# Optimization experiments

Hardware: AMD Instinct MI355X
Metric: run time of the kernel (lower is better)

The kernel has to match this reference:

```python
import jax, jax.numpy as jnp
import numpy as np

B, DIM = 32768, 768
M, K = 128, 32          # num_subvectors, code_size
D = DIM // M            # subvector_dim = 6


def setup_inputs() -> dict:
    key = jax.random.key(0)
    kx, kc = jax.random.split(key)
    x = jax.random.normal(kx, (B, DIM), dtype=jnp.float32)
    codebooks = jax.random.normal(kc, (M, K, D), dtype=jnp.float32) * 0.01
    return {"x": x, "codebooks": codebooks}


def reference(x, codebooks):
    b = x.shape[0]
    m, k, d = codebooks.shape
    sub = x.reshape(b, m, d)                                   # (B, M, D)
    # per-subvector dot products with each code: (B, M, K)
    dots = jnp.einsum('bmd,mkd->bmk', sub, codebooks)
    soft = jax.nn.softmax(dots, axis=2)                        # (B, M, K)
    soft_q = jnp.einsum('bmk,mkd->bmd', soft, codebooks)       # (B, M, D)
    idx = jnp.argmax(dots, axis=2)                             # (B, M) int
    discrete = codebooks[jnp.arange(m)[None, :], idx]          # (B, M, D)
    # straight-through: forward = discrete, gradient flows through soft_q
    quant = soft_q - jax.lax.stop_gradient(soft_q - discrete)
    return quant.reshape(b, m * d)
```

## Files before the change

kernel.cpp:

```cpp
#include <hip/hip_runtime.h>
#include <float.h>


typedef float v2f __attribute__((ext_vector_type(2)));

#define BATCH 32768
#define DIM   768
#define K_CB  32
#define D_SUB 6
#define BROWS 16
#define RSTG  8
#define NSTG  (BROWS/RSTG)
#define HALFF 384
#define STGF  (RSTG*HALFF)

#define DPP_XOR1 0xB1
#define DPP_XOR2 0x4E

template<int CTRL>
__device__ __forceinline__ float dppf(float v) {
    return __int_as_float(__builtin_amdgcn_update_dpp(
        0, __float_as_int(v), CTRL, 0xF, 0xF, true));
}
template<int CTRL>
__device__ __forceinline__ int dppi(int v) {
    return __builtin_amdgcn_update_dpp(0, v, CTRL, 0xF, 0xF, true);
}

__global__ __launch_bounds__(256, 4)
void pq_head_kernel(const float* __restrict__ x,
                    const float* __restrict__ cb,
                    float* __restrict__ out) {
    __shared__ float xs[2][STGF];

    const int t     = threadIdx.x;
    const int kq    = t & 3;
    const int mloc  = t >> 2;
    const int mhalf = blockIdx.y;
    const int m     = mhalf * 64 + mloc;
    const int b0    = blockIdx.x * BROWS;

    v2f cpk[4][D_SUB];
    {
        float cc[48];
        const float4* cb4 = reinterpret_cast<const float4*>(
            cb + ((size_t)m * K_CB + (size_t)kq * 8) * D_SUB);
        #pragma unroll
        for (int i = 0; i < 12; ++i) {
            float4 v = cb4[i];
            cc[4*i+0]=v.x; cc[4*i+1]=v.y; cc[4*i+2]=v.z; cc[4*i+3]=v.w;
        }
        #pragma unroll
        for (int p = 0; p < 4; ++p)
            #pragma unroll
            for (int e = 0; e < D_SUB; ++e)
                cpk[p][e] = (v2f){cc[(2*p)*D_SUB + e], cc[(2*p+1)*D_SUB + e]};
    }

    const float* xh = x   + (size_t)mhalf * HALFF;
    float*       oh = out + (size_t)mhalf * HALFF;

    int pr[3], pc[3];
    #pragma unroll
    for (int i = 0; i < 3; ++i) {
        int f = (i * 256 + t) * 4;
        pr[i] = f / HALFF;
        pc[i] = f - pr[i] * HALFF;
    }

    float4 pf[3];
    #pragma unroll
    for (int i = 0; i < 3; ++i)
        pf[i] = *reinterpret_cast<const float4*>(xh + (size_t)(b0 + pr[i]) * DIM + pc[i]);

    for (int s = 0; s < NSTG; ++s) {
        float* buf = xs[s & 1];
        #pragma unroll
        for (int i = 0; i < 3; ++i)
            *reinterpret_cast<float4*>(&buf[(i * 256 + t) * 4]) = pf[i];
        __syncthreads();

        if (s + 1 < NSTG) {
            int rb = b0 + (s + 1) * RSTG;
            #pragma unroll
            for (int i = 0; i < 3; ++i)
                pf[i] = *reinterpret_cast<const float4*>(
                    xh + (size_t)(rb + pr[i]) * DIM + pc[i]);
        }

        int kg8[RSTG];
        #pragma unroll
        for (int r = 0; r < RSTG; ++r) {
            const float* xr = &buf[r * HALFF + mloc * D_SUB];
            float2 x01 = *reinterpret_cast<const float2*>(xr);
            float2 x23 = *reinterpret_cast<const float2*>(xr + 2);
            float2 x45 = *reinterpret_cast<const float2*>(xr + 4);
            float xv[6] = {x01.x, x01.y, x23.x, x23.y, x45.x, x45.y};
            v2f xxe[6];
            #pragma unroll
            for (int e = 0; e < 6; ++e) xxe[e] = (v2f){xv[e], xv[e]};

            float best1 = -FLT_MAX, best2 = -FLT_MAX;
            int   kg    = kq * 8;
            #pragma unroll
            for (int p = 0; p < 4; ++p) {
                v2f acc = cpk[p][0] * xxe[0];
                #pragma unroll
                for (int e = 1; e < 6; ++e)
                    acc = __builtin_elementwise_fma(cpk[p][e], xxe[e], acc);
                #pragma unroll
                for (int h = 0; h < 2; ++h) {
                    float d  = h ? acc.y : acc.x;
                    bool  gt = d > best1;
                    best2 = gt ? best1 : fmaxf(best2, d);
                    kg    = gt ? (kq * 8 + 2*p + h) : kg;
                    best1 = gt ? d : best1;
                }
            }

            {
                float o1 = dppf<DPP_XOR1>(best1);
                float o2 = dppf<DPP_XOR1>(best2);
                int   ok = dppi<DPP_XOR1>(kg);
                bool take = (o1 > best1) || (o1 == best1 && ok < kg);
                best2 = fmaxf(fminf(best1, o1), fmaxf(best2, o2));
                kg    = take ? ok : kg;
                best1 = fmaxf(best1, o1);
            }
            {
                float o1 = dppf<DPP_XOR2>(best1);
                float o2 = dppf<DPP_XOR2>(best2);
                int   ok = dppi<DPP_XOR2>(kg);
                bool take = (o1 > best1) || (o1 == best1 && ok < kg);
                best2 = fmaxf(fminf(best1, o1), fmaxf(best2, o2));
                kg    = take ? ok : kg;
                best1 = fmaxf(best1, o1);
            }

            if (best1 - best2 < 1e-5f) {
                const float* crow = cb + (size_t)m * K_CB * D_SUB;
                double db = -1e300; int dkg = 0;
                for (int k2 = 0; k2 < K_CB; ++k2) {
                    double sa = 0.0;
                    for (int e = 0; e < 6; ++e)
                        sa = fma((double)crow[k2*6+e], (double)xv[e], sa);
                    if (sa > db) { db = sa; dkg = k2; }
                }
                kg = dkg;
            }
            kg8[r] = kg;
        }

        const bool act = (kq < 3);
        float2 gv[RSTG];
        if (act) {
            #pragma unroll
            for (int r = 0; r < RSTG; ++r)
                gv[r] = *(reinterpret_cast<const float2*>(
                    cb + ((size_t)m * K_CB + (size_t)kg8[r]) * D_SUB) + kq);
        }

        __builtin_amdgcn_sched_barrier(0);

        if (act) {
            #pragma unroll
            for (int r = 0; r < RSTG; ++r) {
                float* dst = oh + (size_t)(b0 + s * RSTG + r) * DIM + mloc * D_SUB;
                *(reinterpret_cast<float2*>(dst) + kq) = gv[r];
            }
        }
    }
}

extern "C" void kernel_launch(void* const* d_in, const int* in_sizes, int n_in,
                              void* d_out, int out_size, void* d_ws, size_t ws_size,
                              hipStream_t stream) {
    const float* x  = (const float*)d_in[0];
    const float* cb = (const float*)d_in[1];
    float* out = (float*)d_out;

    dim3 grid(BATCH / BROWS, 2);
    dim3 block(256);
    hipLaunchKernelGGL(pq_head_kernel, grid, block, 0, stream, x, cb, out);
}
```

Measured before the change: 226.0 us.

## Replace LDS staging with direct per-thread global loads and register double-buffering

Removes the shared-memory staging of x rows and the __syncthreads barriers. Each thread now loads its own 6-float subvector straight from global memory, with a two-row register prefetch, and writes its output gathered one row later. This drops the LDS round trip and the block-wide syncs. The cost is that each float2 global load is less coalesced, since the four lanes of a quad read the same 24 bytes, and there is less memory-level parallelism per thread than the earlier staged 8-row batches gave.

Result: slower. 241.2 us (+6.8%).

```diff
diff --git a/kernel.cpp b/kernel.cpp
--- a/kernel.cpp
+++ b/kernel.cpp
@@ -9,10 +9,7 @@
 #define K_CB  32
 #define D_SUB 6
 #define BROWS 16
-#define RSTG  8
-#define NSTG  (BROWS/RSTG)
 #define HALFF 384
-#define STGF  (RSTG*HALFF)
 
 #define DPP_XOR1 0xB1
 #define DPP_XOR2 0x4E
@@ -31,8 +28,6 @@
 void pq_head_kernel(const float* __restrict__ x,
                     const float* __restrict__ cb,
                     float* __restrict__ out) {
-    __shared__ float xs[2][STGF];
-
     const int t     = threadIdx.x;
     const int kq    = t & 3;
     const int mloc  = t >> 2;
@@ -57,119 +52,95 @@
                 cpk[p][e] = (v2f){cc[(2*p)*D_SUB + e], cc[(2*p+1)*D_SUB + e]};
     }
 
-    const float* xh = x   + (size_t)mhalf * HALFF;
-    float*       oh = out + (size_t)mhalf * HALFF;
+    const float* xb = x   + (size_t)b0 * DIM + (size_t)mhalf * HALFF + mloc * D_SUB;
+    float*       ob = out + (size_t)b0 * DIM + (size_t)mhalf * HALFF + mloc * D_SUB;
 
-    int pr[3], pc[3];
+    const bool act = (kq < 3);
+
+    float2 pfx[2][3];
     #pragma unroll
-    for (int i = 0; i < 3; ++i) {
-        int f = (i * 256 + t) * 4;
-        pr[i] = f / HALFF;
-        pc[i] = f - pr[i] * HALFF;
+    for (int i = 0; i < 2; ++i) {
+        const float2* p = reinterpret_cast<const float2*>(xb + (size_t)i * DIM);
+        pfx[i][0] = p[0]; pfx[i][1] = p[1]; pfx[i][2] = p[2];
     }
 
-    float4 pf[3];
+    float2 gv[2];
+
     #pragma unroll
-    for (int i = 0; i < 3; ++i)
-        pf[i] = *reinterpret_cast<const float4*>(xh + (size_t)(b0 + pr[i]) * DIM + pc[i]);
-
-    for (int s = 0; s < NSTG; ++s) {
-        float* buf = xs[s & 1];
-        #pragma unroll
-        for (int i = 0; i < 3; ++i)
-            *reinterpret_cast<float4*>(&buf[(i * 256 + t) * 4]) = pf[i];
-        __syncthreads();
-
-        if (s + 1 < NSTG) {
-            int rb = b0 + (s + 1) * RSTG;
-            #pragma unroll
-            for (int i = 0; i < 3; ++i)
-                pf[i] = *reinterpret_cast<const float4*>(
-                    xh + (size_t)(rb + pr[i]) * DIM + pc[i]);
+    for (int r = 0; r < BROWS; ++r) {
+        float2 xa = pfx[r & 1][0];
+        float2 xc = pfx[r & 1][1];
+        float2 xe = pfx[r & 1][2];
+        if (r + 2 < BROWS) {
+            const float2* p = reinterpret_cast<const float2*>(xb + (size_t)(r + 2) * DIM);
+            pfx[r & 1][0] = p[0]; pfx[r & 1][1] = p[1]; pfx[r & 1][2] = p[2];
         }
 
-        int kg8[RSTG];
+        float xv[6] = {xa.x, xa.y, xc.x, xc.y, xe.x, xe.y};
+        v2f xxe[6];
         #pragma unroll
-        for (int r = 0; r < RSTG; ++r) {
-            const float* xr = &buf[r * HALFF + mloc * D_SUB];
-            float2 x01 = *reinterpret_cast<const float2*>(xr);
-            float2 x23 = *reinterpret_cast<const float2*>(xr + 2);
-            float2 x45 = *reinterpret_cast<const float2*>(xr + 4);
-            float xv[6] = {x01.x, x01.y, x23.x, x23.y, x45.x, x45.y};
-            v2f xxe[6];
+        for (int e = 0; e < 6; ++e) xxe[e] = (v2f){xv[e], xv[e]};
+
+        float best1 = -FLT_MAX, best2 = -FLT_MAX;
+        int   kg    = kq * 8;
+        #pragma unroll
+        for (int p = 0; p < 4; ++p) {
+            v2f acc = cpk[p][0] * xxe[0];
             #pragma unroll
-            for (int e = 0; e < 6; ++e) xxe[e] = (v2f){xv[e], xv[e]};
-
-            float best1 = -FLT_MAX, best2 = -FLT_MAX;
-            int   kg    = kq * 8;
+            for (int e = 1; e < 6; ++e)
+                acc = __builtin_elementwise_fma(cpk[p][e], xxe[e], acc);
             #pragma unroll
-            for (int p = 0; p < 4; ++p) {
-                v2f acc = cpk[p][0] * xxe[0];
-                #pragma unroll
-                for (int e = 1; e < 6; ++e)
-                    acc = __builtin_elementwise_fma(cpk[p][e], xxe[e], acc);
-                #pragma unroll
-                for (int h = 0; h < 2; ++h) {
-                    float d  = h ? acc.y : acc.x;
-                    bool  gt = d > best1;
-                    best2 = gt ? best1 : fmaxf(best2, d);
-                    kg    = gt ? (kq * 8 + 2*p + h) : kg;
-                    best1 = gt ? d : best1;
-                }
+            for (int h = 0; h < 2; ++h) {
+                float d  = h ? acc.y : acc.x;
+                bool  gt = d > best1;
+                best2 = gt ? best1 : fmaxf(best2, d);
+                kg    = gt ? (kq * 8 + 2*p + h) : kg;
+                best1 = gt ? d : best1;
             }
-
-            {
-                float o1 = dppf<DPP_XOR1>(best1);
-                float o2 = dppf<DPP_XOR1>(best2);
-                int   ok = dppi<DPP_XOR1>(kg);
-                bool take = (o1 > best1) || (o1 == best1 && ok < kg);
-                best2 = fmaxf(fminf(best1, o1), fmaxf(best2, o2));
-                kg    = take ? ok : kg;
-                best1 = fmaxf(best1, o1);
-            }
-            {
-                float o1 = dppf<DPP_XOR2>(best1);
-                float o2 = dppf<DPP_XOR2>(best2);
-                int   ok = dppi<DPP_XOR2>(kg);
-                bool take = (o1 > best1) || (o1 == best1 && ok < kg);
-                best2 = fmaxf(fminf(best1, o1), fmaxf(best2, o2));
-                kg    = take ? ok : kg;
-                best1 = fmaxf(best1, o1);
-            }
-
-            if (best1 - best2 < 1e-5f) {
-                const float* crow = cb + (size_t)m * K_CB * D_SUB;
-                double db = -1e300; int dkg = 0;
-                for (int k2 = 0; k2 < K_CB; ++k2) {
-                    double sa = 0.0;
-                    for (int e = 0; e < 6; ++e)
-                        sa = fma((double)crow[k2*6+e], (double)xv[e], sa);
-                    if (sa > db) { db = sa; dkg = k2; }
-                }
-                kg = dkg;
-            }
-            kg8[r] = kg;
         }
 
-        const bool act = (kq < 3);
-        float2 gv[RSTG];
-        if (act) {
-            #pragma unroll
-            for (int r = 0; r < RSTG; ++r)
-                gv[r] = *(reinterpret_cast<const float2*>(
-                    cb + ((size_t)m * K_CB + (size_t)kg8[r]) * D_SUB) + kq);
+        {
+            float o1 = dppf<DPP_XOR1>(best1);
+            float o2 = dppf<DPP_XOR1>(best2);
+            int   ok = dppi<DPP_XOR1>(kg);
+            bool take = (o1 > best1) || (o1 == best1 && ok < kg);
+            best2 = fmaxf(fminf(best1, o1), fmaxf(best2, o2));
+            kg    = take ? ok : kg;
+            best1 = fmaxf(best1, o1);
+        }
+        {
+            float o1 = dppf<DPP_XOR2>(best1);
+            float o2 = dppf<DPP_XOR2>(best2);
+            int   ok = dppi<DPP_XOR2>(kg);
+            bool take = (o1 > best1) || (o1 == best1 && ok < kg);
+            best2 = fmaxf(fminf(best1, o1), fmaxf(best2, o2));
+            kg    = take ? ok : kg;
+            best1 = fmaxf(best1, o1);
         }
 
-        __builtin_amdgcn_sched_barrier(0);
+        if (best1 - best2 < 1e-5f) {
+            const float* crow = cb + (size_t)m * K_CB * D_SUB;
+            double db = -1e300; int dkg = 0;
+            for (int k2 = 0; k2 < K_CB; ++k2) {
+                double sa = 0.0;
+                for (int e = 0; e < 6; ++e)
+                    sa = fma((double)crow[k2*6+e], (double)xv[e], sa);
+                if (sa > db) { db = sa; dkg = k2; }
+            }
+            kg = dkg;
+        }
 
-        if (act) {
-            #pragma unroll
-            for (int r = 0; r < RSTG; ++r) {
-                float* dst = oh + (size_t)(b0 + s * RSTG + r) * DIM + mloc * D_SUB;
-                *(reinterpret_cast<float2*>(dst) + kq) = gv[r];
-            }
-        }
+        if (act)
+            gv[r & 1] = *(reinterpret_cast<const float2*>(
+                cb + ((size_t)m * K_CB + (size_t)kg) * D_SUB) + kq);
+
+        if (r > 0 && act)
+            *(reinterpret_cast<float2*>(ob + (size_t)(r - 1) * DIM) + kq)
+                = gv[(r - 1) & 1];
     }
+    if (act)
+        *(reinterpret_cast<float2*>(ob + (size_t)(BROWS - 1) * DIM) + kq)
+            = gv[(BROWS - 1) & 1];
 }
 
 extern "C" void kernel_launch(void* const* d_in, const int* in_sizes, int n_in,
```
